# Optimization experiments

Measured on AMD Instinct MI355X. Metric: run time of the kernel, lower is better.

## Reference

```python
import jax, jax.numpy as jnp
import numpy as np

B, C, H, W = 1, 320, 64, 64
HEADS, DH = 8, 40            # inner_dim = 320
CTX_LEN, CTX_DIM = 77, 768
FF_MULT = 4
GN_GROUPS, GN_EPS = 32, 1e-6
LN_EPS = 1e-5
SCALE = DH ** -0.5
WSTD = 0.02


def setup_inputs() -> dict:
    key = jax.random.key(0)
    ks = iter(jax.random.split(key, 32))
    rn = lambda *s: jax.random.normal(next(ks), s, dtype=jnp.float32)
    D = HEADS * DH  # 320
    inp = {
        'hidden_states': rn(B, C, H, W),
        'encoder_hidden_states': rn(B, CTX_LEN, CTX_DIM),
        'gn_g': jnp.ones((C,), jnp.float32), 'gn_b': jnp.zeros((C,), jnp.float32),
        'pi_w': rn(C, D) * WSTD, 'pi_b': jnp.zeros((D,), jnp.float32),
        'n1_g': jnp.ones((D,), jnp.float32), 'n1_b': jnp.zeros((D,), jnp.float32),
        'a1_q': rn(D, D) * WSTD, 'a1_k': rn(D, D) * WSTD, 'a1_v': rn(D, D) * WSTD,
        'a1_o': rn(D, D) * WSTD, 'a1_ob': jnp.zeros((D,), jnp.float32),
        'n2_g': jnp.ones((D,), jnp.float32), 'n2_b': jnp.zeros((D,), jnp.float32),
        'a2_q': rn(D, D) * WSTD, 'a2_k': rn(CTX_DIM, D) * WSTD, 'a2_v': rn(CTX_DIM, D) * WSTD,
        'a2_o': rn(D, D) * WSTD, 'a2_ob': jnp.zeros((D,), jnp.float32),
        'n3_g': jnp.ones((D,), jnp.float32), 'n3_b': jnp.zeros((D,), jnp.float32),
        'ff_w1': rn(D, 2 * FF_MULT * D) * WSTD, 'ff_b1': jnp.zeros((2 * FF_MULT * D,), jnp.float32),
        'ff_w2': rn(FF_MULT * D, D) * WSTD, 'ff_b2': jnp.zeros((D,), jnp.float32),
        'po_w': rn(D, C) * WSTD, 'po_b': jnp.zeros((C,), jnp.float32),
    }
    return inp


def _group_norm(x, g, b):
    # x: [B,C,H,W]
    Bx, Cx, Hx, Wx = x.shape
    xr = x.reshape(Bx, GN_GROUPS, Cx // GN_GROUPS, Hx, Wx)
    mu = xr.mean(axis=(2, 3, 4), keepdims=True)
    var = xr.var(axis=(2, 3, 4), keepdims=True)
    xr = (xr - mu) * jax.lax.rsqrt(var + GN_EPS)
    x = xr.reshape(Bx, Cx, Hx, Wx)
    return x * g[None, :, None, None] + b[None, :, None, None]


def _layer_norm(x, g, b):
    mu = x.mean(-1, keepdims=True)
    var = x.var(-1, keepdims=True)
    return (x - mu) * jax.lax.rsqrt(var + LN_EPS) * g + b


def _attention(x, ctx, wq, wk, wv, wo, bo):
    # x: [B,S,D]; ctx: [B,T,Dc]. Same math as the torch sliced loop
    # (the 2-row slicing changes only execution order, not values).
    Bx, S, D = x.shape
    q = (x @ wq).reshape(Bx, S, HEADS, DH)
    k = (ctx @ wk).reshape(Bx, -1, HEADS, DH)
    v = (ctx @ wv).reshape(Bx, -1, HEADS, DH)
    s = jnp.einsum('bihd,bjhd->bhij', q, k) * SCALE
    p = jax.nn.softmax(s, axis=-1)
    o = jnp.einsum('bhij,bjhd->bihd', p, v).reshape(Bx, S, D)
    return o @ wo + bo


def reference(hidden_states, encoder_hidden_states, gn_g, gn_b, pi_w, pi_b,
              n1_g, n1_b, a1_q, a1_k, a1_v, a1_o, a1_ob,
              n2_g, n2_b, a2_q, a2_k, a2_v, a2_o, a2_ob,
              n3_g, n3_b, ff_w1, ff_b1, ff_w2, ff_b2, po_w, po_b):
    residual = hidden_states
    h = _group_norm(hidden_states, gn_g, gn_b)
    # proj_in: 1x1 conv == per-pixel linear; to [B, HW, D]
    h = jnp.einsum('bchw,cd->bhwd', h, pi_w) + pi_b
    Bx, Hx, Wx, D = h.shape
    h = h.reshape(Bx, Hx * Wx, D)

    # transformer block
    nh = _layer_norm(h, n1_g, n1_b)
    h = h + _attention(nh, nh, a1_q, a1_k, a1_v, a1_o, a1_ob)
    nh = _layer_norm(h, n2_g, n2_b)
    h = h + _attention(nh, encoder_hidden_states, a2_q, a2_k, a2_v, a2_o, a2_ob)
    nh = _layer_norm(h, n3_g, n3_b)
    hg = nh @ ff_w1 + ff_b1
    a, gate = jnp.split(hg, 2, axis=-1)  # GEGLU
    h = h + (a * jax.nn.gelu(gate, approximate=False)) @ ff_w2 + ff_b2

    # proj_out 1x1 conv then residual
    h = h.reshape(Bx, Hx, Wx, D)
    out = jnp.einsum('bhwd,dc->bchw', h, po_w) + po_b[None, :, None, None]
    return out + residual
```

## Files before the change

kernel.cpp:

```cpp
#include <hip/hip_runtime.h>

typedef __bf16 bf16x8 __attribute__((ext_vector_type(8)));
typedef __bf16 bf16x4 __attribute__((ext_vector_type(4)));
typedef float f32x4 __attribute__((ext_vector_type(4)));

#define MFMA16(a, b, c) __builtin_amdgcn_mfma_f32_16x16x32_bf16(a, b, c, 0, 0, 0)

static constexpr float QSCALE = 0.15811388300841897f * 1.4426950408889634f;

__device__ __forceinline__ void gload16(const __bf16* g, __bf16* l) {
  __builtin_amdgcn_global_load_lds((const __attribute__((address_space(1))) void*)g,
                                   (__attribute__((address_space(3))) void*)l, 16, 0, 0);
}

__device__ __forceinline__ bf16x8 zero8() {
  bf16x8 z;
#pragma unroll
  for (int j = 0; j < 8; ++j) z[j] = (__bf16)0.0f;
  return z;
}

__device__ __forceinline__ float gelu_exact(float x) {
  return 0.5f * x * (1.0f + erff(x * 0.70710678118654752f));
}

__device__ __forceinline__ int vperm(int lo) {
  return (lo & 35) | ((lo & 12) << 1) | ((lo & 16) >> 2);
}

struct WDesc { const float* src; __bf16* dst; int K; int N; int ldn; int noff; };
struct WTable { WDesc w[12]; };

__global__ __launch_bounds__(256) void wconv_kernel(WTable tab) {
  WDesc d = tab.w[blockIdx.y];
  int total = (d.K >> 3) * d.N;
  int idx = blockIdx.x * 256 + threadIdx.x;
  if (idx >= total) return;
  int kb = idx / d.N, n = idx - kb * d.N;
  bf16x8 o;
#pragma unroll
  for (int j = 0; j < 8; ++j) o[j] = (__bf16)d.src[(size_t)(kb * 8 + j) * d.N + n];
  *(bf16x8*)&d.dst[((size_t)kb * d.ldn + d.noff + n) * 8] = o;
}

__global__ __launch_bounds__(256) void gn_stats(const float* __restrict__ X,
                                                float* __restrict__ part) {
  int g = blockIdx.x >> 3, cid = blockIdx.x & 7;
  const float* base = X + (size_t)g * 40960 + (size_t)cid * 5120;
  int t = threadIdx.x;
  float s = 0.f, s2 = 0.f;
#pragma unroll
  for (int i = t; i < 1280; i += 256) {
    float4 v = ((const float4*)base)[i];
    s += v.x + v.y + v.z + v.w;
    s2 += v.x * v.x + v.y * v.y + v.z * v.z + v.w * v.w;
  }
#pragma unroll
  for (int off = 1; off < 64; off <<= 1) { s += __shfl_xor(s, off); s2 += __shfl_xor(s2, off); }
  __shared__ float rs[4], rs2[4];
  int wid = t >> 6, lane = t & 63;
  if (lane == 0) { rs[wid] = s; rs2[wid] = s2; }
  __syncthreads();
  if (t == 0) {
    part[blockIdx.x * 2] = rs[0] + rs[1] + rs[2] + rs[3];
    part[blockIdx.x * 2 + 1] = rs2[0] + rs2[1] + rs2[2] + rs2[3];
  }
}

__global__ __launch_bounds__(256) void gn_apply(const float* __restrict__ X,
                                                const float* __restrict__ part,
                                                const float* __restrict__ gg,
                                                const float* __restrict__ gb,
                                                __bf16* __restrict__ Y) {
  int i0 = (blockIdx.x * 256 + threadIdx.x) * 8;
  int c = i0 >> 12, px = i0 & 4095;
  int g = c / 10;
  float s = 0.f, s2 = 0.f;
#pragma unroll
  for (int j = 0; j < 8; ++j) { s += part[(g * 8 + j) * 2]; s2 += part[(g * 8 + j) * 2 + 1]; }
  float mu = s * (1.f / 40960.f);
  float rstd = rsqrtf(s2 * (1.f / 40960.f) - mu * mu + 1e-6f);
  float ga = gg[c] * rstd, bb = gb[c] - mu * ga;
  float4 a = *(const float4*)&X[i0];
  float4 b = *(const float4*)&X[i0 + 4];
  Y[(size_t)(px + 0) * 320 + c] = (__bf16)(a.x * ga + bb);
  Y[(size_t)(px + 1) * 320 + c] = (__bf16)(a.y * ga + bb);
  Y[(size_t)(px + 2) * 320 + c] = (__bf16)(a.z * ga + bb);
  Y[(size_t)(px + 3) * 320 + c] = (__bf16)(a.w * ga + bb);
  Y[(size_t)(px + 4) * 320 + c] = (__bf16)(b.x * ga + bb);
  Y[(size_t)(px + 5) * 320 + c] = (__bf16)(b.y * ga + bb);
  Y[(size_t)(px + 6) * 320 + c] = (__bf16)(b.z * ga + bb);
  Y[(size_t)(px + 7) * 320 + c] = (__bf16)(b.w * ga + bb);
}

__global__ __launch_bounds__(256) void ln_kernel(const float* __restrict__ X,
                                                 const float* __restrict__ g,
                                                 const float* __restrict__ b,
                                                 __bf16* __restrict__ Y) {
  int row = blockIdx.x * 4 + (threadIdx.x >> 6);
  int lane = threadIdx.x & 63;
  const float* x = X + (size_t)row * 320;
  float v[5];
  float s = 0.f;
#pragma unroll
  for (int i = 0; i < 5; ++i) { v[i] = x[lane + 64 * i]; s += v[i]; }
#pragma unroll
  for (int off = 1; off < 64; off <<= 1) s += __shfl_xor(s, off);
  float mu = s * (1.f / 320.f);
  float s2 = 0.f;
#pragma unroll
  for (int i = 0; i < 5; ++i) { float d = v[i] - mu; s2 += d * d; }
#pragma unroll
  for (int off = 1; off < 64; off <<= 1) s2 += __shfl_xor(s2, off);
  float rstd = rsqrtf(s2 * (1.f / 320.f) + 1e-5f);
#pragma unroll
  for (int i = 0; i < 5; ++i) {
    int c = lane + 64 * i;
    Y[(size_t)row * 320 + c] = (__bf16)((v[i] - mu) * rstd * g[c] + b[c]);
  }
}

template <int OM, bool HB, bool HR, bool QS, bool AH>
__global__ __launch_bounds__(256) void gemm64(const __bf16* __restrict__ A,
                                              const __bf16* __restrict__ Bt,
                                              const float* __restrict__ bias,
                                              const float* __restrict__ res,
                                              void* __restrict__ Cout,
                                              void* __restrict__ Cout2,
                                              int M, int N, int K) {
  __shared__ __align__(16) __bf16 sA[2][4096];
  __shared__ __align__(16) __bf16 sB[2][4096];
  int t = threadIdx.x, lane = t & 63, wid = t >> 6;
  int wr = wid >> 1, wc = wid & 1, kb4 = lane >> 4, l15 = lane & 15;
  int m0 = blockIdx.x * 64, n0 = blockIdx.y * 64;
  const size_t N8 = (size_t)N * 8;
  f32x4 acc[2][2] = {};
  int r0 = t >> 3, c0 = (t & 7) ^ (r0 & 7);

  auto stage = [&](int buf, int k0) {
    const __bf16 *ga0, *ga1;
    if (AH) {
      int kk = k0 + c0 * 8;
      int hh = kk / 40, dh = kk - hh * 40;
      ga0 = &A[((size_t)hh * 4096 + m0 + r0) * 40 + dh];
      ga1 = &A[((size_t)hh * 4096 + m0 + 32 + r0) * 40 + dh];
    } else {
      ga0 = &A[(size_t)(m0 + r0) * K + k0 + c0 * 8];
      ga1 = &A[(size_t)(m0 + 32 + r0) * K + k0 + c0 * 8];
    }
    gload16(ga0, &sA[buf][wid * 512]);
    gload16(ga1, &sA[buf][2048 + wid * 512]);
    gload16(&Bt[((size_t)(k0 >> 3) + wid) * N8 + (size_t)(n0 + lane) * 8], &sB[buf][wid * 512]);
    gload16(&Bt[((size_t)(k0 >> 3) + wid + 4) * N8 + (size_t)(n0 + lane) * 8], &sB[buf][2048 + wid * 512]);
  };
  stage(0, 0);
  __syncthreads();
  int cur = 0;
  for (int k0 = 0; k0 < K; k0 += 64) {
    if (k0 + 64 < K) stage(cur ^ 1, k0 + 64);
#pragma unroll
    for (int kk = 0; kk < 2; ++kk) {
      int c8 = kb4 + kk * 4;
      bf16x8 af[2], bfr[2];
#pragma unroll
      for (int fm = 0; fm < 2; ++fm) {
        int row = wr * 32 + fm * 16 + l15;
        af[fm] = *(const bf16x8*)&sA[cur][row * 64 + ((c8 * 8) ^ ((row & 7) << 3))];
      }
#pragma unroll
      for (int fn = 0; fn < 2; ++fn)
        bfr[fn] = *(const bf16x8*)&sB[cur][(c8 * 64 + wc * 32 + fn * 16 + l15) * 8];
#pragma unroll
      for (int fm = 0; fm < 2; ++fm)
#pragma unroll
        for (int fn = 0; fn < 2; ++fn) acc[fm][fn] = MFMA16(af[fm], bfr[fn], acc[fm][fn]);
    }
    __syncthreads();
    cur ^= 1;
  }
#pragma unroll
  for (int fm = 0; fm < 2; ++fm)
#pragma unroll
    for (int fn = 0; fn < 2; ++fn)
#pragma unroll
      for (int r = 0; r < 4; ++r) {
        int row = m0 + wr * 32 + fm * 16 + kb4 * 4 + r;
        int col = n0 + wc * 32 + fn * 16 + l15;
        float v = acc[fm][fn][r];
        if (HB) v += bias[col];
        if (OM == 3) {
          if (HR) v += res[(size_t)col * M + row];
          ((float*)Cout)[(size_t)col * M + row] = v;
        } else if (OM == 4) {
          int hh = col / 40, dh = col - hh * 40;
          ((__bf16*)Cout)[((size_t)hh * 4096 + row) * 40 + dh] = (__bf16)(QS ? v * QSCALE : v);
        } else {
          if (HR) v += res[(size_t)row * N + col];
          if (OM == 0) {
            ((float*)Cout)[(size_t)row * N + col] = v;
          } else if (OM == 1) {
            ((__bf16*)Cout)[(size_t)row * N + col] = (__bf16)(QS ? v * QSCALE : v);
          } else {
            ((float*)Cout)[(size_t)row * N + col] = v;
            ((__bf16*)Cout2)[(size_t)row * N + col] = (__bf16)v;
          }
        }
      }
}

__global__ __launch_bounds__(256) void qkv_gemm(const __bf16* __restrict__ A,
                                                const __bf16* __restrict__ Bt,
                                                __bf16* __restrict__ Qh,
                                                __bf16* __restrict__ Kh,
                                                __bf16* __restrict__ Vt) {
  __shared__ __align__(16) __bf16 sA[2][4096];
  __shared__ __align__(16) __bf16 sB[2][4096];
  int t = threadIdx.x, lane = t & 63, wid = t >> 6;
  int wr = wid >> 1, wc = wid & 1, kb4 = lane >> 4, l15 = lane & 15;
  int m0 = blockIdx.x * 64, n0 = blockIdx.y * 64;
  f32x4 acc[2][2] = {};
  int r0 = t >> 3, c0 = (t & 7) ^ (r0 & 7);

  auto stage = [&](int buf, int k0) {
    gload16(&A[(size_t)(m0 + r0) * 320 + k0 + c0 * 8], &sA[buf][wid * 512]);
    gload16(&A[(size_t)(m0 + 32 + r0) * 320 + k0 + c0 * 8], &sA[buf][2048 + wid * 512]);
    gload16(&Bt[((size_t)(k0 >> 3) + wid) * (960 * 8) + (size_t)(n0 + lane) * 8], &sB[buf][wid * 512]);
    gload16(&Bt[((size_t)(k0 >> 3) + wid + 4) * (960 * 8) + (size_t)(n0 + lane) * 8], &sB[buf][2048 + wid * 512]);
  };
  stage(0, 0);
  __syncthreads();
  int cur = 0;
  for (int k0 = 0; k0 < 320; k0 += 64) {
    if (k0 + 64 < 320) stage(cur ^ 1, k0 + 64);
#pragma unroll
    for (int kk = 0; kk < 2; ++kk) {
      int c8 = kb4 + kk * 4;
      bf16x8 af[2], bfr[2];
#pragma unroll
      for (int fm = 0; fm < 2; ++fm) {
        int row = wr * 32 + fm * 16 + l15;
        af[fm] = *(const bf16x8*)&sA[cur][row * 64 + ((c8 * 8) ^ ((row & 7) << 3))];
      }
#pragma unroll
      for (int fn = 0; fn < 2; ++fn)
        bfr[fn] = *(const bf16x8*)&sB[cur][(c8 * 64 + wc * 32 + fn * 16 + l15) * 8];
#pragma unroll
      for (int fm = 0; fm < 2; ++fm)
#pragma unroll
        for (int fn = 0; fn < 2; ++fn) acc[fm][fn] = MFMA16(af[fm], bfr[fn], acc[fm][fn]);
    }
    __syncthreads();
    cur ^= 1;
  }
#pragma unroll
  for (int fm = 0; fm < 2; ++fm)
#pragma unroll
    for (int fn = 0; fn < 2; ++fn)
#pragma unroll
      for (int r = 0; r < 4; ++r) {
        int row = m0 + wr * 32 + fm * 16 + kb4 * 4 + r;
        int col = n0 + wc * 32 + fn * 16 + l15;
        float v = acc[fm][fn][r];
        if (col < 320) {
          int hh = col / 40, dh = col - hh * 40;
          Qh[((size_t)hh * 4096 + row) * 40 + dh] = (__bf16)(v * QSCALE);
        } else if (col < 640) {
          int d = col - 320;
          int hh = d / 40, dh = d - hh * 40;
          Kh[((size_t)hh * 4096 + row) * 40 + dh] = (__bf16)v;
        } else {
          int d = col - 640;
          int jj = vperm(row & 63) ^ ((d & 7) << 3);
          Vt[(size_t)d * 4096 + (row & ~63) + jj] = (__bf16)v;
        }
      }
}

__global__ __launch_bounds__(256) void kv2_gemm(const float* __restrict__ Af,
                                                const __bf16* __restrict__ Bt,
                                                __bf16* __restrict__ Kh,
                                                __bf16* __restrict__ Vt) {
  __shared__ __align__(16) __bf16 sA[2][4][64][8];
  __shared__ __align__(16) __bf16 sB[2][4][64][8];
  int t = threadIdx.x, lane = t & 63, wid = t >> 6;
  int wr = wid >> 1, wc = wid & 1, kb4 = lane >> 4, l15 = lane & 15;
  int m0 = blockIdx.x * 64, n0 = blockIdx.y * 64;
  int am = t & 63, ac8 = t >> 6;
  int bn = t & 63, bkb = t >> 6;
  f32x4 acc[2][2] = {};
  bf16x8 rA, rB;
  auto loadA = [&](int k0) -> bf16x8 {
    if (m0 + am < 77) {
      const float* src = &Af[(size_t)(m0 + am) * 768 + k0 + ac8 * 8];
      float4 x = *(const float4*)src;
      float4 y = *(const float4*)(src + 4);
      bf16x8 o;
      o[0] = (__bf16)x.x; o[1] = (__bf16)x.y; o[2] = (__bf16)x.z; o[3] = (__bf16)x.w;
      o[4] = (__bf16)y.x; o[5] = (__bf16)y.y; o[6] = (__bf16)y.z; o[7] = (__bf16)y.w;
      return o;
    }
    return zero8();
  };
  auto loadB = [&](int k0) {
    return *(const bf16x8*)&Bt[((size_t)(k0 >> 3) + bkb) * (640 * 8) + (size_t)(n0 + bn) * 8];
  };
  rA = loadA(0); rB = loadB(0);
  *(bf16x8*)&sA[0][ac8][am][0] = rA;
  *(bf16x8*)&sB[0][bkb][bn][0] = rB;
  __syncthreads();
  int cur = 0;
  for (int k0 = 0; k0 < 768; k0 += 32, cur ^= 1) {
    bool more = (k0 + 32) < 768;
    if (more) { rA = loadA(k0 + 32); rB = loadB(k0 + 32); }
    bf16x8 af[2], bfr[2];
#pragma unroll
    for (int fm = 0; fm < 2; ++fm) af[fm] = *(const bf16x8*)&sA[cur][kb4][wr * 32 + fm * 16 + l15][0];
#pragma unroll
    for (int fn = 0; fn < 2; ++fn) bfr[fn] = *(const bf16x8*)&sB[cur][kb4][wc * 32 + fn * 16 + l15][0];
#pragma unroll
    for (int fm = 0; fm < 2; ++fm)
#pragma unroll
      for (int fn = 0; fn < 2; ++fn) acc[fm][fn] = MFMA16(af[fm], bfr[fn], acc[fm][fn]);
    if (more) {
      *(bf16x8*)&sA[cur ^ 1][ac8][am][0] = rA;
      *(bf16x8*)&sB[cur ^ 1][bkb][bn][0] = rB;
    }
    __syncthreads();
  }
#pragma unroll
  for (int fm = 0; fm < 2; ++fm)
#pragma unroll
    for (int fn = 0; fn < 2; ++fn)
#pragma unroll
      for (int r = 0; r < 4; ++r) {
        int row = m0 + wr * 32 + fm * 16 + kb4 * 4 + r;
        int col = n0 + wc * 32 + fn * 16 + l15;
        float v = acc[fm][fn][r];
        if (col < 320) {
          int hh = col / 40, dh = col - hh * 40;
          Kh[((size_t)hh * 128 + row) * 40 + dh] = (__bf16)v;
        } else {
          int d = col - 320;
          int jj = vperm(row & 63) ^ ((d & 7) << 3);
          Vt[(size_t)d * 128 + (row & ~63) + jj] = (__bf16)v;
        }
      }
}

__global__ __launch_bounds__(256) void geglu64(const __bf16* __restrict__ A,
                                               const __bf16* __restrict__ Bt,
                                               const float* __restrict__ bias,
                                               __bf16* __restrict__ Out) {
  __shared__ __align__(16) __bf16 sA[2][4096];
  __shared__ __align__(16) __bf16 sB[2][4096];
  __shared__ __align__(16) __bf16 sBg[2][4096];
  int t = threadIdx.x, lane = t & 63, wid = t >> 6;
  int wr = wid >> 1, wc = wid & 1, kb4 = lane >> 4, l15 = lane & 15;
  int m0 = blockIdx.x * 64, n0 = blockIdx.y * 64;
  f32x4 acc_a[2][2] = {}, acc_g[2][2] = {};
  int r0 = t >> 3, c0 = (t & 7) ^ (r0 & 7);

  auto stage = [&](int buf, int k0) {
    gload16(&A[(size_t)(m0 + r0) * 320 + k0 + c0 * 8], &sA[buf][wid * 512]);
    gload16(&A[(size_t)(m0 + 32 + r0) * 320 + k0 + c0 * 8], &sA[buf][2048 + wid * 512]);
    gload16(&Bt[((size_t)(k0 >> 3) + wid) * (2560 * 8) + (size_t)(n0 + lane) * 8], &sB[buf][wid * 512]);
    gload16(&Bt[((size_t)(k0 >> 3) + wid + 4) * (2560 * 8) + (size_t)(n0 + lane) * 8], &sB[buf][2048 + wid * 512]);
    gload16(&Bt[((size_t)(k0 >> 3) + wid) * (2560 * 8) + (size_t)(1280 + n0 + lane) * 8], &sBg[buf][wid * 512]);
    gload16(&Bt[((size_t)(k0 >> 3) + wid + 4) * (2560 * 8) + (size_t)(1280 + n0 + lane) * 8], &sBg[buf][2048 + wid * 512]);
  };
  stage(0, 0);
  __syncthreads();
  int cur = 0;
  for (int k0 = 0; k0 < 320; k0 += 64) {
    if (k0 + 64 < 320) stage(cur ^ 1, k0 + 64);
#pragma unroll
    for (int kk = 0; kk < 2; ++kk) {
      int c8 = kb4 + kk * 4;
      bf16x8 af[2], bfa[2], bfg[2];
#pragma unroll
      for (int fm = 0; fm < 2; ++fm) {
        int row = wr * 32 + fm * 16 + l15;
        af[fm] = *(const bf16x8*)&sA[cur][row * 64 + ((c8 * 8) ^ ((row & 7) << 3))];
      }
#pragma unroll
      for (int fn = 0; fn < 2; ++fn) {
        bfa[fn] = *(const bf16x8*)&sB[cur][(c8 * 64 + wc * 32 + fn * 16 + l15) * 8];
        bfg[fn] = *(const bf16x8*)&sBg[cur][(c8 * 64 + wc * 32 + fn * 16 + l15) * 8];
      }
#pragma unroll
      for (int fm = 0; fm < 2; ++fm)
#pragma unroll
        for (int fn = 0; fn < 2; ++fn) {
          acc_a[fm][fn] = MFMA16(af[fm], bfa[fn], acc_a[fm][fn]);
          acc_g[fm][fn] = MFMA16(af[fm], bfg[fn], acc_g[fm][fn]);
        }
    }
    __syncthreads();
    cur ^= 1;
  }
#pragma unroll
  for (int fm = 0; fm < 2; ++fm)
#pragma unroll
    for (int fn = 0; fn < 2; ++fn)
#pragma unroll
      for (int r = 0; r < 4; ++r) {
        int row = m0 + wr * 32 + fm * 16 + kb4 * 4 + r;
        int col = n0 + wc * 32 + fn * 16 + l15;
        float a = acc_a[fm][fn][r] + bias[col];
        float g = acc_g[fm][fn][r] + bias[1280 + col];
        Out[(size_t)row * 1280 + col] = (__bf16)(a * gelu_exact(g));
      }
}

__global__ __launch_bounds__(512) void attn_kernel(const __bf16* __restrict__ Qh,
                                                   const __bf16* __restrict__ Kh,
                                                   const __bf16* __restrict__ Vt,
                                                   __bf16* __restrict__ Oh,
                                                   int kv_len, int kvpad, int vt_stride,
                                                   int half) {
  __shared__ __align__(16) __bf16 sK[2][2][2560];
  __shared__ __align__(16) __bf16 sV[2][2][3072];
  __shared__ __align__(16) float sO[3072];
  int t = threadIdx.x, lane = t & 63, wid = t >> 6;
  int grp = wid >> 2, wsub = wid & 3, tl = t & 255;
  int kb4 = lane >> 4, l15 = lane & 15;
  int h = blockIdx.y, q0 = blockIdx.x * 64;
  int q = q0 + wsub * 16 + l15;

  for (int i = t; i < 2048; i += 512) {
    int g = i >> 10, b = (i >> 9) & 1, j = i & 511;
    sV[g][b][2560 + j] = (j < 64) ? (__bf16)1.0f : (__bf16)0.0f;
  }

  const __bf16* Kbase = Kh + (size_t)h * kvpad * 40;
  const __bf16* Vbase = Vt + (size_t)h * 40 * vt_stride;

  bf16x8 qf0, qf1;
  {
    const __bf16* qrow = Qh + ((size_t)h * 4096 + q) * 40;
    qf0 = *(const bf16x8*)(qrow + kb4 * 8);
    qf1 = (kb4 == 0) ? *(const bf16x8*)(qrow + 32) : zero8();
  }
  f32x4 o_f[3] = {};

  auto stage = [&](int buf, int k0) {
    gload16(Kbase + (size_t)k0 * 40 + tl * 8, &sK[grp][buf][wsub * 512]);
    gload16(Vbase + (size_t)(tl >> 3) * vt_stride + k0 + (tl & 7) * 8, &sV[grp][buf][wsub * 512]);
    if (tl < 64) {
      gload16(Kbase + (size_t)k0 * 40 + 2048 + lane * 8, &sK[grp][buf][2048]);
      gload16(Vbase + (size_t)(32 + (lane >> 3)) * vt_stride + k0 + (lane & 7) * 8, &sV[grp][buf][2048]);
    }
  };

  int kstart = grp * half;
  int ntiles = half >> 6;
  stage(0, kstart);
  __syncthreads();
  for (int tile = 0; tile < ntiles; ++tile) {
    int k0 = kstart + (tile << 6), cur = tile & 1;
    if (tile + 1 < ntiles) stage(cur ^ 1, k0 + 64);
    const __bf16* K8 = &sK[grp][cur][0];
    f32x4 s[4];
#pragma unroll
    for (int cf = 0; cf < 4; ++cf) {
      int key = cf * 16 + l15;
      bf16x8 kf0 = *(const bf16x8*)&K8[key * 40 + kb4 * 8];
      bf16x8 kf1 = *(const bf16x8*)&K8[key * 40 + 32];
      f32x4 z = {0.f, 0.f, 0.f, 0.f};
      z = MFMA16(kf0, qf0, z);
      s[cf] = MFMA16(kf1, qf1, z);
    }
    if (k0 + 64 > kv_len) {
#pragma unroll
      for (int cf = 0; cf < 4; ++cf)
#pragma unroll
        for (int r = 0; r < 4; ++r)
          if (k0 + cf * 16 + kb4 * 4 + r >= kv_len) s[cf][r] = -1e30f;
    }
    bf16x8 p0, p1;
#pragma unroll
    for (int j = 0; j < 8; ++j) {
      p0[j] = (__bf16)exp2f(s[j >> 2][j & 3]);
      p1[j] = (__bf16)exp2f(s[2 + (j >> 2)][j & 3]);
    }
    const __bf16* V8 = &sV[grp][cur][0];
#pragma unroll
    for (int f = 0; f < 3; ++f) {
      int dd = f * 16 + l15;
      int sw = (dd & 7) << 3;
      bf16x8 v0 = *(const bf16x8*)&V8[dd * 64 + ((kb4 * 8) ^ sw)];
      bf16x8 v1 = *(const bf16x8*)&V8[dd * 64 + ((32 + kb4 * 8) ^ sw)];
      o_f[f] = MFMA16(v0, p0, o_f[f]);
      o_f[f] = MFMA16(v1, p1, o_f[f]);
    }
    __syncthreads();
  }
  if (grp == 1) {
    float* dst = &sO[tl * 12];
#pragma unroll
    for (int f = 0; f < 3; ++f)
#pragma unroll
      for (int r = 0; r < 4; ++r) dst[f * 4 + r] = o_f[f][r];
  }
  __syncthreads();
  if (grp == 0) {
    const float* src = &sO[tl * 12];
#pragma unroll
    for (int f = 0; f < 3; ++f)
#pragma unroll
      for (int r = 0; r < 4; ++r) o_f[f][r] += src[f * 4 + r];
    float lsum = __shfl(o_f[2][0], 32 + l15);
    float inv = 1.0f / lsum;
    __bf16* orow = Oh + ((size_t)h * 4096 + q) * 40;
#pragma unroll
    for (int f = 0; f < 3; ++f) {
      int d0 = f * 16 + kb4 * 4;
      if (d0 < 40) {
        bf16x4 o4;
#pragma unroll
        for (int r = 0; r < 4; ++r) o4[r] = (__bf16)(o_f[f][r] * inv);
        *(bf16x4*)(orow + d0) = o4;
      }
    }
  }
}

extern "C" void kernel_launch(void* const* d_in, const int* in_sizes, int n_in,
                              void* d_out, int out_size, void* d_ws, size_t ws_size,
                              hipStream_t stream) {
  const float* hs    = (const float*)d_in[0];
  const float* ctx   = (const float*)d_in[1];
  const float* gn_g  = (const float*)d_in[2];
  const float* gn_b  = (const float*)d_in[3];
  const float* pi_w  = (const float*)d_in[4];
  const float* pi_b  = (const float*)d_in[5];
  const float* n1_g  = (const float*)d_in[6];
  const float* n1_b  = (const float*)d_in[7];
  const float* a1_q  = (const float*)d_in[8];
  const float* a1_k  = (const float*)d_in[9];
  const float* a1_v  = (const float*)d_in[10];
  const float* a1_o  = (const float*)d_in[11];
  const float* a1_ob = (const float*)d_in[12];
  const float* n2_g  = (const float*)d_in[13];
  const float* n2_b  = (const float*)d_in[14];
  const float* a2_q  = (const float*)d_in[15];
  const float* a2_k  = (const float*)d_in[16];
  const float* a2_v  = (const float*)d_in[17];
  const float* a2_o  = (const float*)d_in[18];
  const float* a2_ob = (const float*)d_in[19];
  const float* n3_g  = (const float*)d_in[20];
  const float* n3_b  = (const float*)d_in[21];
  const float* ff_w1 = (const float*)d_in[22];
  const float* ff_b1 = (const float*)d_in[23];
  const float* ff_w2 = (const float*)d_in[24];
  const float* ff_b2 = (const float*)d_in[25];
  const float* po_w  = (const float*)d_in[26];
  const float* po_b  = (const float*)d_in[27];

  char* p = (char*)d_ws;
  auto alloc = [&](size_t bytes) {
    char* r = p;
    p += (bytes + 255) & ~(size_t)255;
    return r;
  };
  __bf16* wPI  = (__bf16*)alloc((size_t)320 * 320 * 2);
  __bf16* wQKV = (__bf16*)alloc((size_t)320 * 960 * 2);
  __bf16* wO1  = (__bf16*)alloc((size_t)320 * 320 * 2);
  __bf16* wQ2  = (__bf16*)alloc((size_t)320 * 320 * 2);
  __bf16* wKV2 = (__bf16*)alloc((size_t)768 * 640 * 2);
  __bf16* wO2  = (__bf16*)alloc((size_t)320 * 320 * 2);
  __bf16* wFF1 = (__bf16*)alloc((size_t)320 * 2560 * 2);
  __bf16* wFF2 = (__bf16*)alloc((size_t)1280 * 320 * 2);
  __bf16* wPO  = (__bf16*)alloc((size_t)320 * 320 * 2);

  float*  gpart= (float*)alloc((size_t)256 * 2 * 4);
  __bf16* xg   = (__bf16*)alloc((size_t)4096 * 320 * 2);
  float*  h    = (float*)alloc((size_t)4096 * 320 * 4);
  __bf16* hb   = (__bf16*)alloc((size_t)4096 * 320 * 2);
  __bf16* nx   = (__bf16*)alloc((size_t)4096 * 320 * 2);
  __bf16* qh   = (__bf16*)alloc((size_t)4096 * 320 * 2);
  __bf16* kh   = (__bf16*)alloc((size_t)4096 * 320 * 2);
  __bf16* vt   = (__bf16*)alloc((size_t)320 * 4096 * 2);
  __bf16* kh2  = (__bf16*)alloc((size_t)8 * 128 * 40 * 2);
  __bf16* vt2  = (__bf16*)alloc((size_t)320 * 128 * 2);
  __bf16* oh   = (__bf16*)alloc((size_t)4096 * 320 * 2);
  __bf16* g    = (__bf16*)alloc((size_t)4096 * 1280 * 2);
  float*  outp = (float*)d_out;

  WTable tab;
  tab.w[0]  = WDesc{pi_w,  wPI,  320, 320, 320, 0};
  tab.w[1]  = WDesc{a1_q,  wQKV, 320, 320, 960, 0};
  tab.w[2]  = WDesc{a1_k,  wQKV, 320, 320, 960, 320};
  tab.w[3]  = WDesc{a1_v,  wQKV, 320, 320, 960, 640};
  tab.w[4]  = WDesc{a1_o,  wO1,  320, 320, 320, 0};
  tab.w[5]  = WDesc{a2_q,  wQ2,  320, 320, 320, 0};
  tab.w[6]  = WDesc{a2_k,  wKV2, 768, 320, 640, 0};
  tab.w[7]  = WDesc{a2_v,  wKV2, 768, 320, 640, 320};
  tab.w[8]  = WDesc{a2_o,  wO2,  320, 320, 320, 0};
  tab.w[9]  = WDesc{ff_w1, wFF1, 320, 2560, 2560, 0};
  tab.w[10] = WDesc{ff_w2, wFF2, 1280, 320, 320, 0};
  tab.w[11] = WDesc{po_w,  wPO,  320, 320, 320, 0};
  wconv_kernel<<<dim3(400, 12), 256, 0, stream>>>(tab);
  gn_stats<<<dim3(256), 256, 0, stream>>>(hs, gpart);
  gn_apply<<<dim3(640), 256, 0, stream>>>(hs, gpart, gn_g, gn_b, xg);
  gemm64<0, true, false, false, false><<<dim3(64, 5), 256, 0, stream>>>(xg, wPI, pi_b, nullptr, h, nullptr, 4096, 320, 320);
  ln_kernel<<<dim3(1024), 256, 0, stream>>>(h, n1_g, n1_b, nx);
  qkv_gemm<<<dim3(64, 15), 256, 0, stream>>>(nx, wQKV, qh, kh, vt);
  attn_kernel<<<dim3(64, 8), 512, 0, stream>>>(qh, kh, vt, oh, 4096, 4096, 4096, 2048);
  gemm64<0, true, true, false, true><<<dim3(64, 5), 256, 0, stream>>>(oh, wO1, a1_ob, h, h, nullptr, 4096, 320, 320);
  ln_kernel<<<dim3(1024), 256, 0, stream>>>(h, n2_g, n2_b, nx);
  gemm64<4, false, false, true, false><<<dim3(64, 5), 256, 0, stream>>>(nx, wQ2, nullptr, nullptr, qh, nullptr, 4096, 320, 320);
  kv2_gemm<<<dim3(2, 10), 256, 0, stream>>>(ctx, wKV2, kh2, vt2);
  attn_kernel<<<dim3(64, 8), 512, 0, stream>>>(qh, kh2, vt2, oh, 77, 128, 128, 64);
  gemm64<0, true, true, false, true><<<dim3(64, 5), 256, 0, stream>>>(oh, wO2, a2_ob, h, h, nullptr, 4096, 320, 320);
  ln_kernel<<<dim3(1024), 256, 0, stream>>>(h, n3_g, n3_b, nx);
  geglu64<<<dim3(64, 20), 256, 0, stream>>>(nx, wFF1, ff_b1, g);
  gemm64<2, true, true, false, false><<<dim3(64, 5), 256, 0, stream>>>(g, wFF2, ff_b2, h, h, hb, 4096, 320, 1280);
  gemm64<3, true, true, false, false><<<dim3(64, 5), 256, 0, stream>>>(hb, wPO, po_b, hs, outp, nullptr, 4096, 320, 320);
}
```

Baseline: 185.1 us.

## Rewrite attention with 32x32 MFMA, padded Q/K head dim, tiled V layout

Rewrites the attention kernel to use 32x32x16 bf16 MFMA instead of 16x16x32. Q and K are stored padded from head dim 40 to 48 so the K-dimension splits into three slices. V is written by the producer GEMMs in a per-tile swizzled layout, and the row-sum is obtained from a constant ones block. Work is split four ways across key ranges and query halves, with an LDS reduction at the end. The change targets MFMA instruction count and wasted padding in the softmax-free attention, at the cost of extra padded memory and a larger final reduction.

```diff
diff --git a/kernel.cpp b/kernel.cpp
--- a/kernel.cpp
+++ b/kernel.cpp
@@ -2,9 +2,12 @@
 
 typedef __bf16 bf16x8 __attribute__((ext_vector_type(8)));
 typedef __bf16 bf16x4 __attribute__((ext_vector_type(4)));
+typedef __bf16 bf16x2 __attribute__((ext_vector_type(2)));
 typedef float f32x4 __attribute__((ext_vector_type(4)));
+typedef float f32x16 __attribute__((ext_vector_type(16)));
 
 #define MFMA16(a, b, c) __builtin_amdgcn_mfma_f32_16x16x32_bf16(a, b, c, 0, 0, 0)
+#define MFMA32(a, b, c) __builtin_amdgcn_mfma_f32_32x32x16_bf16(a, b, c, 0, 0, 0)
 
 static constexpr float QSCALE = 0.15811388300841897f * 1.4426950408889634f;
 
@@ -24,8 +27,11 @@
   return 0.5f * x * (1.0f + erff(x * 0.70710678118654752f));
 }
 
-__device__ __forceinline__ int vperm(int lo) {
-  return (lo & 35) | ((lo & 12) << 1) | ((lo & 16) >> 2);
+__device__ __forceinline__ int vslot(int kk) {
+  int G = kk >> 5, klo = kk & 31;
+  int m = (klo >> 4) & 1, hik = (klo >> 2) & 1;
+  int jj = (klo & 3) | (((klo >> 3) & 1) << 2);
+  return (G << 5) | (m << 4) | (hik << 3) | jj;
 }
 
 struct WDesc { const float* src; __bf16* dst; int K; int N; int ldn; int noff; };
@@ -193,7 +199,9 @@
           ((float*)Cout)[(size_t)col * M + row] = v;
         } else if (OM == 4) {
           int hh = col / 40, dh = col - hh * 40;
-          ((__bf16*)Cout)[((size_t)hh * 4096 + row) * 40 + dh] = (__bf16)(QS ? v * QSCALE : v);
+          __bf16* qp = (__bf16*)Cout + ((size_t)hh * 4096 + row) * 48 + dh;
+          *qp = (__bf16)(QS ? v * QSCALE : v);
+          if (dh >= 32) qp[8] = (__bf16)0.f;
         } else {
           if (HR) v += res[(size_t)row * N + col];
           if (OM == 0) {
@@ -211,8 +219,8 @@
 __global__ __launch_bounds__(256) void qkv_gemm(const __bf16* __restrict__ A,
                                                 const __bf16* __restrict__ Bt,
                                                 __bf16* __restrict__ Qh,
-                                                __bf16* __restrict__ Kh,
-                                                __bf16* __restrict__ Vt) {
+                                                __bf16* __restrict__ Khp,
+                                                __bf16* __restrict__ Vtl) {
   __shared__ __align__(16) __bf16 sA[2][4096];
   __shared__ __align__(16) __bf16 sB[2][4096];
   int t = threadIdx.x, lane = t & 63, wid = t >> 6;
@@ -263,23 +271,30 @@
         float v = acc[fm][fn][r];
         if (col < 320) {
           int hh = col / 40, dh = col - hh * 40;
-          Qh[((size_t)hh * 4096 + row) * 40 + dh] = (__bf16)(v * QSCALE);
+          __bf16* qp = &Qh[((size_t)hh * 4096 + row) * 48 + dh];
+          *qp = (__bf16)(v * QSCALE);
+          if (dh >= 32) qp[8] = (__bf16)0.f;
         } else if (col < 640) {
           int d = col - 320;
           int hh = d / 40, dh = d - hh * 40;
-          Kh[((size_t)hh * 4096 + row) * 40 + dh] = (__bf16)v;
+          __bf16* kp = &Khp[((size_t)hh * 4096 + row) * 48 + dh];
+          *kp = (__bf16)v;
+          if (dh >= 32) kp[8] = (__bf16)0.f;
         } else {
           int d = col - 640;
-          int jj = vperm(row & 63) ^ ((d & 7) << 3);
-          Vt[(size_t)d * 4096 + (row & ~63) + jj] = (__bf16)v;
+          int hh = d / 40, dh = d - hh * 40;
+          int kt = row >> 6;
+          int slot = vslot(row & 63);
+          int cidx = (slot & 7) | ((((slot >> 3) ^ dh) & 7) << 3);
+          Vtl[(((size_t)hh * 64 + kt) * 40 + dh) * 64 + cidx] = (__bf16)v;
         }
       }
 }
 
 __global__ __launch_bounds__(256) void kv2_gemm(const float* __restrict__ Af,
                                                 const __bf16* __restrict__ Bt,
-                                                __bf16* __restrict__ Kh,
-                                                __bf16* __restrict__ Vt) {
+                                                __bf16* __restrict__ Khp,
+                                                __bf16* __restrict__ Vtl) {
   __shared__ __align__(16) __bf16 sA[2][4][64][8];
   __shared__ __align__(16) __bf16 sB[2][4][64][8];
   int t = threadIdx.x, lane = t & 63, wid = t >> 6;
@@ -338,11 +353,16 @@
         float v = acc[fm][fn][r];
         if (col < 320) {
           int hh = col / 40, dh = col - hh * 40;
-          Kh[((size_t)hh * 128 + row) * 40 + dh] = (__bf16)v;
+          __bf16* kp = &Khp[((size_t)hh * 128 + row) * 48 + dh];
+          *kp = (__bf16)v;
+          if (dh >= 32) kp[8] = (__bf16)0.f;
         } else {
           int d = col - 320;
-          int jj = vperm(row & 63) ^ ((d & 7) << 3);
-          Vt[(size_t)d * 128 + (row & ~63) + jj] = (__bf16)v;
+          int hh = d / 40, dh = d - hh * 40;
+          int kt = row >> 6;
+          int slot = vslot(row & 63);
+          int cidx = (slot & 7) | ((((slot >> 3) ^ dh) & 7) << 3);
+          Vtl[(((size_t)hh * 2 + kt) * 40 + dh) * 64 + cidx] = (__bf16)v;
         }
       }
 }
@@ -413,114 +433,127 @@
 }
 
 __global__ __launch_bounds__(512) void attn_kernel(const __bf16* __restrict__ Qh,
-                                                   const __bf16* __restrict__ Kh,
-                                                   const __bf16* __restrict__ Vt,
+                                                   const __bf16* __restrict__ Khp,
+                                                   const __bf16* __restrict__ Vtl,
                                                    __bf16* __restrict__ Oh,
-                                                   int kv_len, int kvpad, int vt_stride,
-                                                   int half) {
-  __shared__ __align__(16) __bf16 sK[2][2][2560];
-  __shared__ __align__(16) __bf16 sV[2][2][3072];
-  __shared__ __align__(16) float sO[3072];
+                                                   int kv_len, int kvpad) {
+  __shared__ __align__(16) char smem[48128];
   int t = threadIdx.x, lane = t & 63, wid = t >> 6;
-  int grp = wid >> 2, wsub = wid & 3, tl = t & 255;
-  int kb4 = lane >> 4, l15 = lane & 15;
+  int zz = wid >> 2, kg = (wid >> 1) & 1, qg = wid & 1;
+  int tl = t & 255, wv = wid & 3;
+  int l31 = lane & 31, hi = lane >> 5;
   int h = blockIdx.y, q0 = blockIdx.x * 64;
-  int q = q0 + wsub * 16 + l15;
-
-  for (int i = t; i < 2048; i += 512) {
-    int g = i >> 10, b = (i >> 9) & 1, j = i & 511;
-    sV[g][b][2560 + j] = (j < 64) ? (__bf16)1.0f : (__bf16)0.0f;
-  }
-
-  const __bf16* Kbase = Kh + (size_t)h * kvpad * 40;
-  const __bf16* Vbase = Vt + (size_t)h * 40 * vt_stride;
-
-  bf16x8 qf0, qf1;
+  int q = q0 + qg * 32 + l31;
+  int NT = kvpad >> 6;
+  char* zbase = smem + zz * 22528;
+  __bf16* sK  = (__bf16*)zbase;
+  __bf16* sVs = (__bf16*)(zbase + 12288);
+  __bf16* sVc = (__bf16*)(smem + 45056);
+  for (int i = t; i < 1536; i += 512) sVc[i] = (i < 64) ? (__bf16)1.0f : (__bf16)0.0f;
+
+  const __bf16* Kb = Khp + (size_t)h * kvpad * 48;
+  const __bf16* Vb = Vtl + (size_t)h * NT * 2560;
+
+  bf16x8 qf[3];
   {
-    const __bf16* qrow = Qh + ((size_t)h * 4096 + q) * 40;
-    qf0 = *(const bf16x8*)(qrow + kb4 * 8);
-    qf1 = (kb4 == 0) ? *(const bf16x8*)(qrow + 32) : zero8();
-  }
-  f32x4 o_f[3] = {};
+    const __bf16* qrow = Qh + ((size_t)h * 4096 + q) * 48;
+#pragma unroll
+    for (int s = 0; s < 3; ++s) qf[s] = *(const bf16x8*)(qrow + s * 16 + hi * 8);
+  }
+  f32x16 o_lo = {}, o_hi = {};
 
   auto stage = [&](int buf, int k0) {
-    gload16(Kbase + (size_t)k0 * 40 + tl * 8, &sK[grp][buf][wsub * 512]);
-    gload16(Vbase + (size_t)(tl >> 3) * vt_stride + k0 + (tl & 7) * 8, &sV[grp][buf][wsub * 512]);
-    if (tl < 64) {
-      gload16(Kbase + (size_t)k0 * 40 + 2048 + lane * 8, &sK[grp][buf][2048]);
-      gload16(Vbase + (size_t)(32 + (lane >> 3)) * vt_stride + k0 + (lane & 7) * 8, &sV[grp][buf][2048]);
-    }
+    const __bf16* kgp = Kb + (size_t)k0 * 48;
+    __bf16* kd = sK + buf * 3072;
+    gload16(kgp + tl * 8, kd + wv * 512);
+    if (tl < 128) gload16(kgp + 2048 + tl * 8, kd + 2048 + wv * 512);
+    const __bf16* vgp = Vb + (size_t)(k0 >> 6) * 2560;
+    __bf16* vd = sVs + buf * 2560;
+    gload16(vgp + tl * 8, vd + wv * 512);
+    if (tl < 64) gload16(vgp + 2048 + tl * 8, vd + 2048);
   };
 
-  int kstart = grp * half;
-  int ntiles = half >> 6;
+  int span = kvpad >> 1;
+  int kstart = zz * span, ntl = span >> 6;
   stage(0, kstart);
   __syncthreads();
-  for (int tile = 0; tile < ntiles; ++tile) {
+  int d7 = l31 & 7;
+  for (int tile = 0; tile < ntl; ++tile) {
     int k0 = kstart + (tile << 6), cur = tile & 1;
-    if (tile + 1 < ntiles) stage(cur ^ 1, k0 + 64);
-    const __bf16* K8 = &sK[grp][cur][0];
-    f32x4 s[4];
-#pragma unroll
-    for (int cf = 0; cf < 4; ++cf) {
-      int key = cf * 16 + l15;
-      bf16x8 kf0 = *(const bf16x8*)&K8[key * 40 + kb4 * 8];
-      bf16x8 kf1 = *(const bf16x8*)&K8[key * 40 + 32];
-      f32x4 z = {0.f, 0.f, 0.f, 0.f};
-      z = MFMA16(kf0, qf0, z);
-      s[cf] = MFMA16(kf1, qf1, z);
+    if (tile + 1 < ntl) stage(cur ^ 1, k0 + 64);
+    const __bf16* K8 = sK + cur * 3072 + (kg * 32 + l31) * 48 + hi * 8;
+    f32x16 s = {};
+#pragma unroll
+    for (int sl = 0; sl < 3; ++sl) {
+      bf16x8 kf = *(const bf16x8*)(K8 + sl * 16);
+      s = MFMA32(kf, qf[sl], s);
     }
     if (k0 + 64 > kv_len) {
 #pragma unroll
-      for (int cf = 0; cf < 4; ++cf)
-#pragma unroll
-        for (int r = 0; r < 4; ++r)
-          if (k0 + cf * 16 + kb4 * 4 + r >= kv_len) s[cf][r] = -1e30f;
+      for (int r = 0; r < 16; ++r) {
+        int klo = (r & 3) + 8 * (r >> 2) + 4 * hi;
+        if (k0 + kg * 32 + klo >= kv_len) s[r] = -1e30f;
+      }
     }
     bf16x8 p0, p1;
 #pragma unroll
     for (int j = 0; j < 8; ++j) {
-      p0[j] = (__bf16)exp2f(s[j >> 2][j & 3]);
-      p1[j] = (__bf16)exp2f(s[2 + (j >> 2)][j & 3]);
-    }
-    const __bf16* V8 = &sV[grp][cur][0];
-#pragma unroll
-    for (int f = 0; f < 3; ++f) {
-      int dd = f * 16 + l15;
-      int sw = (dd & 7) << 3;
-      bf16x8 v0 = *(const bf16x8*)&V8[dd * 64 + ((kb4 * 8) ^ sw)];
-      bf16x8 v1 = *(const bf16x8*)&V8[dd * 64 + ((32 + kb4 * 8) ^ sw)];
-      o_f[f] = MFMA16(v0, p0, o_f[f]);
-      o_f[f] = MFMA16(v1, p1, o_f[f]);
+      p0[j] = (__bf16)exp2f(s[j]);
+      p1[j] = (__bf16)exp2f(s[8 + j]);
+    }
+    const __bf16* Vlo = sVs + cur * 2560 + l31 * 64;
+    const __bf16* Vhi = (l31 < 8) ? (sVs + cur * 2560 + (32 + l31) * 64)
+                                  : (sVc + (l31 - 8) * 64);
+#pragma unroll
+    for (int m = 0; m < 2; ++m) {
+      int blk = (4 * kg + 2 * m + hi) ^ d7;
+      bf16x8 vlo = *(const bf16x8*)(Vlo + blk * 8);
+      bf16x8 vhi = *(const bf16x8*)(Vhi + blk * 8);
+      bf16x8 pm = (m == 0) ? p0 : p1;
+      o_lo = MFMA32(vlo, pm, o_lo);
+      o_hi = MFMA32(vhi, pm, o_hi);
     }
     __syncthreads();
   }
-  if (grp == 1) {
-    float* dst = &sO[tl * 12];
-#pragma unroll
-    for (int f = 0; f < 3; ++f)
-#pragma unroll
-      for (int r = 0; r < 4; ++r) dst[f * 4 + r] = o_f[f][r];
+  float* sO = (float*)smem;
+  int srcid = zz * 2 + kg;
+  if (srcid != 0) {
+    float* dst = sO + (((size_t)qg * 3 + (srcid - 1)) * 64 + lane) * 24;
+#pragma unroll
+    for (int r = 0; r < 16; ++r) dst[r] = o_lo[r];
+#pragma unroll
+    for (int r = 0; r < 4; ++r) dst[16 + r] = o_hi[r];
+    dst[20] = o_hi[4];
   }
   __syncthreads();
-  if (grp == 0) {
-    const float* src = &sO[tl * 12];
-#pragma unroll
-    for (int f = 0; f < 3; ++f)
-#pragma unroll
-      for (int r = 0; r < 4; ++r) o_f[f][r] += src[f * 4 + r];
-    float lsum = __shfl(o_f[2][0], 32 + l15);
-    float inv = 1.0f / lsum;
+  if (srcid == 0) {
+#pragma unroll
+    for (int src = 0; src < 3; ++src) {
+      const float* sp = sO + (((size_t)qg * 3 + src) * 64 + lane) * 24;
+#pragma unroll
+      for (int r = 0; r < 16; ++r) o_lo[r] += sp[r];
+#pragma unroll
+      for (int r = 0; r < 4; ++r) o_hi[r] += sp[16 + r];
+      o_hi[4] += sp[20];
+    }
+    float ls = __shfl(o_hi[4], l31);
+    float inv = 1.0f / ls;
     __bf16* orow = Oh + ((size_t)h * 4096 + q) * 40;
 #pragma unroll
-    for (int f = 0; f < 3; ++f) {
-      int d0 = f * 16 + kb4 * 4;
-      if (d0 < 40) {
-        bf16x4 o4;
-#pragma unroll
-        for (int r = 0; r < 4; ++r) o4[r] = (__bf16)(o_f[f][r] * inv);
-        *(bf16x4*)(orow + d0) = o4;
-      }
+    for (int r = 0; r < 16; r += 2) {
+      int d = (r & 3) + 8 * (r >> 2) + 4 * hi;
+      bf16x2 o2;
+      o2[0] = (__bf16)(o_lo[r] * inv);
+      o2[1] = (__bf16)(o_lo[r + 1] * inv);
+      *(bf16x2*)(orow + d) = o2;
+    }
+#pragma unroll
+    for (int r = 0; r < 4; r += 2) {
+      int d = 32 + r + 4 * hi;
+      bf16x2 o2;
+      o2[0] = (__bf16)(o_hi[r] * inv);
+      o2[1] = (__bf16)(o_hi[r + 1] * inv);
+      *(bf16x2*)(orow + d) = o2;
     }
   }
 }
@@ -578,11 +611,11 @@
   float*  h    = (float*)alloc((size_t)4096 * 320 * 4);
   __bf16* hb   = (__bf16*)alloc((size_t)4096 * 320 * 2);
   __bf16* nx   = (__bf16*)alloc((size_t)4096 * 320 * 2);
-  __bf16* qh   = (__bf16*)alloc((size_t)4096 * 320 * 2);
-  __bf16* kh   = (__bf16*)alloc((size_t)4096 * 320 * 2);
-  __bf16* vt   = (__bf16*)alloc((size_t)320 * 4096 * 2);
-  __bf16* kh2  = (__bf16*)alloc((size_t)8 * 128 * 40 * 2);
-  __bf16* vt2  = (__bf16*)alloc((size_t)320 * 128 * 2);
+  __bf16* qh   = (__bf16*)alloc((size_t)8 * 4096 * 48 * 2);
+  __bf16* khp  = (__bf16*)alloc((size_t)8 * 4096 * 48 * 2);
+  __bf16* vtl  = (__bf16*)alloc((size_t)8 * 64 * 2560 * 2);
+  __bf16* kh2  = (__bf16*)alloc((size_t)8 * 128 * 48 * 2);
+  __bf16* vt2  = (__bf16*)alloc((size_t)8 * 2 * 2560 * 2);
   __bf16* oh   = (__bf16*)alloc((size_t)4096 * 320 * 2);
   __bf16* g    = (__bf16*)alloc((size_t)4096 * 1280 * 2);
   float*  outp = (float*)d_out;
@@ -605,13 +638,13 @@
   gn_apply<<<dim3(640), 256, 0, stream>>>(hs, gpart, gn_g, gn_b, xg);
   gemm64<0, true, false, false, false><<<dim3(64, 5), 256, 0, stream>>>(xg, wPI, pi_b, nullptr, h, nullptr, 4096, 320, 320);
   ln_kernel<<<dim3(1024), 256, 0, stream>>>(h, n1_g, n1_b, nx);
-  qkv_gemm<<<dim3(64, 15), 256, 0, stream>>>(nx, wQKV, qh, kh, vt);
-  attn_kernel<<<dim3(64, 8), 512, 0, stream>>>(qh, kh, vt, oh, 4096, 4096, 4096, 2048);
+  qkv_gemm<<<dim3(64, 15), 256, 0, stream>>>(nx, wQKV, qh, khp, vtl);
+  attn_kernel<<<dim3(64, 8), 512, 0, stream>>>(qh, khp, vtl, oh, 4096, 4096);
   gemm64<0, true, true, false, true><<<dim3(64, 5), 256, 0, stream>>>(oh, wO1, a1_ob, h, h, nullptr, 4096, 320, 320);
   ln_kernel<<<dim3(1024), 256, 0, stream>>>(h, n2_g, n2_b, nx);
   gemm64<4, false, false, true, false><<<dim3(64, 5), 256, 0, stream>>>(nx, wQ2, nullptr, nullptr, qh, nullptr, 4096, 320, 320);
   kv2_gemm<<<dim3(2, 10), 256, 0, stream>>>(ctx, wKV2, kh2, vt2);
-  attn_kernel<<<dim3(64, 8), 512, 0, stream>>>(qh, kh2, vt2, oh, 77, 128, 128, 64);
+  attn_kernel<<<dim3(64, 8), 512, 0, stream>>>(qh, kh2, vt2, oh, 77, 128);
   gemm64<0, true, true, false, true><<<dim3(64, 5), 256, 0, stream>>>(oh, wO2, a2_ob, h, h, nullptr, 4096, 320, 320);
   ln_kernel<<<dim3(1024), 256, 0, stream>>>(h, n3_g, n3_b, nx);
   geglu64<<<dim3(64, 20), 256, 0, stream>>>(nx, wFF1, ff_b1, g);
```

After: 177.5 us. 1.04x faster.
